# Kernel optimization log

Measured on AMD Instinct MI355X. Metric: run time of the kernel, lower is better.

The kernel has to match this reference:

```python
import jax, jax.numpy as jnp
import numpy as np
import math

B, S, D, H = 4, 2048, 1024, 16
DK = D // H  # 64
THETA = 10000.0


def setup_inputs() -> dict:
    key = jax.random.key(0)
    ks = jax.random.split(key, 5)
    std = 0.02
    return {
        "x": jax.random.normal(ks[0], (B, S, D), dtype=jnp.float32),
        "Wq": jax.random.normal(ks[1], (D, D), dtype=jnp.float32) * std,
        "Wk": jax.random.normal(ks[2], (D, D), dtype=jnp.float32) * std,
        "Wv": jax.random.normal(ks[3], (D, D), dtype=jnp.float32) * std,
        "Wo": jax.random.normal(ks[4], (D, D), dtype=jnp.float32) * std / math.sqrt(2 * 12),
        "token_positions": jnp.arange(S, dtype=jnp.int32),
    }


def _rope(x, pos):
    # x: [B, H, S, DK]; pos: [S]. Interleaved-pair rotary embedding.
    inv_freq = THETA ** (-jnp.arange(0, DK, 2, dtype=jnp.float32) / DK)  # [DK/2]
    ang = pos.astype(jnp.float32)[:, None] * inv_freq[None, :]  # [S, DK/2]
    cos, sin = jnp.cos(ang), jnp.sin(ang)
    x1, x2 = x[..., 0::2], x[..., 1::2]  # [B, H, S, DK/2]
    r1 = x1 * cos - x2 * sin
    r2 = x1 * sin + x2 * cos
    return jnp.stack([r1, r2], axis=-1).reshape(x.shape)


def reference(x, Wq, Wk, Wv, Wo, token_positions):
    b, s, d = x.shape
    Q = x @ Wq
    K = x @ Wk
    V = x @ Wv
    # [B, S, D] -> [B, H, S, DK]
    def split(t):
        return t.reshape(b, s, H, DK).transpose(0, 2, 1, 3)
    Qh, Kh, Vh = split(Q), split(K), split(V)
    Qh = _rope(Qh, token_positions)
    Kh = _rope(Kh, token_positions)
    scores = jnp.einsum('bhqd,bhkd->bhqk', Qh, Kh) / math.sqrt(DK)
    causal = jnp.tril(jnp.ones((s, s), dtype=bool))
    scores = jnp.where(causal, scores, -jnp.inf)
    probs = jax.nn.softmax(scores, axis=-1)
    out = jnp.einsum('bhqk,bhkd->bhqd', probs, Vh)
    out = out.transpose(0, 2, 1, 3).reshape(b, s, d)
    return out @ Wo
```

## Files before the change

### kernel.cpp

```cpp
#include <hip/hip_runtime.h>
#include <hip/hip_bf16.h>

#define B_N 4
#define S_LEN 2048
#define D_MODEL 1024
#define N_HEAD 16
#define D_HEAD 64
#define M_ROWS (B_N * S_LEN)

typedef short bf16x8 __attribute__((ext_vector_type(8)));
typedef short bf16x4 __attribute__((ext_vector_type(4)));
typedef float f32x4 __attribute__((ext_vector_type(4)));

#if __has_builtin(__builtin_amdgcn_mfma_f32_16x16x16bf16_1k)
#define HAVE_MFMA16 1
#else
#define HAVE_MFMA16 0
#endif

__device__ __forceinline__ unsigned short f2bf(float f) {
  union { float f; unsigned int u; } v; v.f = f;
  unsigned int r = v.u + 0x7FFFu + ((v.u >> 16) & 1u);
  return (unsigned short)(r >> 16);
}
__device__ __forceinline__ float bf2f(unsigned short u) {
  union { unsigned int u; float f; } v; v.u = ((unsigned int)u) << 16;
  return v.f;
}
__device__ __forceinline__ unsigned int pkbf(float a, float b) {
  union { __hip_bfloat162 h; unsigned int u; } cv;
  cv.h = __float22bfloat162_rn(make_float2(a, b));
  return cv.u;
}
__device__ __forceinline__ bf16x8 ld8(const unsigned short* p) {
  return *reinterpret_cast<const bf16x8*>(p);
}
__device__ __forceinline__ bf16x4 ld4(const unsigned short* p) {
  return *reinterpret_cast<const bf16x4*>(p);
}
__device__ __forceinline__ void glds16(const unsigned short* g, unsigned short* l) {
  __builtin_amdgcn_global_load_lds(
      (const __attribute__((address_space(1))) unsigned int*)g,
      (__attribute__((address_space(3))) unsigned int*)l, 16, 0, 0);
}

__global__ __launch_bounds__(256) void rope_tab_k(const int* __restrict__ pos,
                                                  float2* __restrict__ tab) {
  const int idx = blockIdx.x * 256 + threadIdx.x;
  const int s = idx >> 5;
  const int i = idx & 31;
  const float inv = exp2f(-(float)i * 0.41524101186092029f);
  const float ang = (float)pos[s] * inv;
  tab[idx] = make_float2(cosf(ang), sinf(ang));
}

__global__ __launch_bounds__(256) void cast_k(const float* __restrict__ X,
                                              unsigned short* __restrict__ Y) {
  const size_t i = ((size_t)blockIdx.x * 256 + threadIdx.x) * 8;
  const float4 a = *reinterpret_cast<const float4*>(X + i);
  const float4 b = *reinterpret_cast<const float4*>(X + i + 4);
  union { unsigned int u[4]; uint4 v; } o;
  o.u[0] = pkbf(a.x, a.y); o.u[1] = pkbf(a.z, a.w);
  o.u[2] = pkbf(b.x, b.y); o.u[3] = pkbf(b.z, b.w);
  *reinterpret_cast<uint4*>(Y + i) = o.v;
}

__global__ __launch_bounds__(256) void wtrans_k(
    const float* __restrict__ W0, const float* __restrict__ W1,
    const float* __restrict__ W2, const float* __restrict__ W3,
    unsigned short* __restrict__ T0, unsigned short* __restrict__ T1,
    unsigned short* __restrict__ T2, unsigned short* __restrict__ T3) {
  const int z = blockIdx.z;
  const float* __restrict__ W = (z == 0) ? W0 : (z == 1) ? W1 : (z == 2) ? W2 : W3;
  unsigned short* __restrict__ T = (z == 0) ? T0 : (z == 1) ? T1 : (z == 2) ? T2 : T3;
  __shared__ __align__(16) unsigned short tile[64][72];
  const int kb = blockIdx.x * 64;
  const int nb = blockIdx.y * 64;
#pragma unroll
  for (int it = 0; it < 2; ++it) {
    const int chunk = it * 256 + threadIdx.x;
    const int r = chunk >> 3;
    const int c8 = (chunk & 7) * 8;
    const float* src = W + (size_t)(kb + r) * D_MODEL + nb + c8;
    const float4 a = *reinterpret_cast<const float4*>(src);
    const float4 b = *reinterpret_cast<const float4*>(src + 4);
    union { unsigned int u[4]; uint4 v; } o;
    o.u[0] = pkbf(a.x, a.y); o.u[1] = pkbf(a.z, a.w);
    o.u[2] = pkbf(b.x, b.y); o.u[3] = pkbf(b.z, b.w);
    *reinterpret_cast<uint4*>(&tile[r][c8]) = o.v;
  }
  __syncthreads();
#pragma unroll
  for (int it = 0; it < 2; ++it) {
    const int chunk = it * 256 + threadIdx.x;
    const int n = chunk >> 3;
    const int k8 = (chunk & 7) * 8;
    __align__(16) unsigned short vals[8];
#pragma unroll
    for (int j = 0; j < 8; ++j) vals[j] = tile[k8 + j][n];
    *reinterpret_cast<uint4*>(T + (size_t)(nb + n) * D_MODEL + kb + k8) =
        *reinterpret_cast<const uint4*>(vals);
  }
}

__global__ __launch_bounds__(256) void gemm2_k(
    const unsigned short* __restrict__ A, const unsigned short* __restrict__ W,
    unsigned short* __restrict__ Qo, unsigned short* __restrict__ Ko,
    unsigned short* __restrict__ VTo, float* __restrict__ OF,
    const float2* __restrict__ tab, const int mode) {
  __shared__ __align__(16) unsigned short smem[4][64][68];
  unsigned short* As = &smem[0][0][0];
  unsigned short* Bs = As + 128 * 32;

  const int tid = threadIdx.x;
  const int lane = tid & 63;
  const int w = tid >> 6;
  const int l15 = lane & 15;
  const int l4 = lane >> 4;

  const int row0 = blockIdx.x * 128;
  const int col0 = blockIdx.y * 128;

  const int srow = w * 32 + (lane >> 2);
  const int scol = (lane & 3) * 8;
  const unsigned short* ga = A + (size_t)(row0 + srow) * D_MODEL + scol;
  const unsigned short* gb = W + (size_t)(col0 + srow) * D_MODEL + scol;
  unsigned short* la = &As[(w * 32) * 32];
  unsigned short* lb = &Bs[(w * 32) * 32];

  const int wrow = (w & 1) * 64;
  const int wcol = (w >> 1) * 64;

  f32x4 acc[4][4];
  const f32x4 fz = {0.f, 0.f, 0.f, 0.f};
#pragma unroll
  for (int m = 0; m < 4; ++m)
#pragma unroll
    for (int n = 0; n < 4; ++n) acc[m][n] = fz;

  for (int kb = 0; kb < D_MODEL; kb += 32) {
    glds16(ga + kb, la);
    glds16(ga + 16 * D_MODEL + kb, la + 16 * 32);
    glds16(gb + kb, lb);
    glds16(gb + 16 * D_MODEL + kb, lb + 16 * 32);
    __syncthreads();
    bf16x8 af[4], bfr[4];
#pragma unroll
    for (int m = 0; m < 4; ++m) af[m] = ld8(&As[(wrow + m * 16 + l15) * 32 + l4 * 8]);
#pragma unroll
    for (int n = 0; n < 4; ++n) bfr[n] = ld8(&Bs[(wcol + n * 16 + l15) * 32 + l4 * 8]);
#pragma unroll
    for (int m = 0; m < 4; ++m)
#pragma unroll
      for (int n = 0; n < 4; ++n)
        acc[m][n] = __builtin_amdgcn_mfma_f32_16x16x32_bf16(af[m], bfr[n], acc[m][n], 0, 0, 0);
    __syncthreads();
  }

  if (mode == 1) {
#pragma unroll
    for (int n = 0; n < 4; ++n) {
      const int gcol = col0 + wcol + n * 16 + l15;
#pragma unroll
      for (int m = 0; m < 4; ++m)
#pragma unroll
        for (int r = 0; r < 4; ++r)
          OF[(size_t)(row0 + wrow + m * 16 + l4 * 4 + r) * D_MODEL + gcol] = acc[m][n][r];
    }
    return;
  }

  unsigned short (*T)[68] = (unsigned short(*)[68]) & smem[w];
  const bool isV = (col0 >= 2048);
  if (!isV) {
#pragma unroll
    for (int m = 0; m < 4; ++m)
#pragma unroll
      for (int n = 0; n < 4; ++n)
#pragma unroll
        for (int r = 0; r < 4; ++r)
          T[m * 16 + l4 * 4 + r][n * 16 + l15] = f2bf(acc[m][n][r]);
  } else {
#pragma unroll
    for (int m = 0; m < 4; ++m)
#pragma unroll
      for (int n = 0; n < 4; ++n)
#pragma unroll
        for (int r = 0; r < 4; ++r)
          T[n * 16 + l15][m * 16 + l4 * 4 + r] = f2bf(acc[m][n][r]);
  }

  const int lr = lane >> 3;
  const int lc = lane & 7;
  if (!isV) {
    const bool isQ = (col0 < 1024);
    unsigned short* O = isQ ? Qo : Ko;
    const float qs = isQ ? 0.18033688011112042f : 1.0f;
    const int cbase = (col0 & 1023) + wcol;
#pragma unroll
    for (int rg = 0; rg < 8; ++rg) {
      const int trow = rg * 8 + lr;
      const int grow = row0 + wrow + trow;
      const int s = grow & (S_LEN - 1);
      const bf16x8 vv = ld8(&T[trow][lc * 8]);
      const float4 tA = *reinterpret_cast<const float4*>(&tab[s * 32 + lc * 4]);
      const float4 tB = *reinterpret_cast<const float4*>(&tab[s * 32 + lc * 4 + 2]);
      float x[8];
#pragma unroll
      for (int j = 0; j < 8; ++j) x[j] = bf2f((unsigned short)vv[j]);
      union { unsigned int u[4]; uint4 v; } o;
      o.u[0] = pkbf((x[0] * tA.x - x[1] * tA.y) * qs, (x[0] * tA.y + x[1] * tA.x) * qs);
      o.u[1] = pkbf((x[2] * tA.z - x[3] * tA.w) * qs, (x[2] * tA.w + x[3] * tA.z) * qs);
      o.u[2] = pkbf((x[4] * tB.x - x[5] * tB.y) * qs, (x[4] * tB.y + x[5] * tB.x) * qs);
      o.u[3] = pkbf((x[6] * tB.z - x[7] * tB.w) * qs, (x[6] * tB.w + x[7] * tB.z) * qs);
      *reinterpret_cast<uint4*>(O + (size_t)grow * D_MODEL + cbase + lc * 8) = o.v;
    }
  } else {
    const int vc0 = (col0 - 2048) + wcol;
    const int h = vc0 >> 6;
    const int b = row0 >> 11;
    const int s0 = (row0 & (S_LEN - 1)) + wrow;
#pragma unroll
    for (int rg = 0; rg < 8; ++rg) {
      const int dk = rg * 8 + lr;
      const bf16x8 vv = ld8(&T[dk][lc * 8]);
      *reinterpret_cast<bf16x8*>(
          VTo + ((size_t)((b << 4) + h) * 64 + dk) * S_LEN + s0 + lc * 8) = vv;
    }
  }
}

__global__ __launch_bounds__(512) void attn6_k(
    const unsigned short* __restrict__ Q, const unsigned short* __restrict__ K,
    const unsigned short* __restrict__ VT, unsigned short* __restrict__ O) {
  const int pair = blockIdx.x;
  const int h = blockIdx.y;
  const int b = blockIdx.z;
  const int tid = threadIdx.x;
  const int w = tid >> 6;
  const int lane = tid & 63;
  const int l15 = lane & 15;
  const int l4 = lane >> 4;

  __shared__ __align__(16) unsigned short Ks[64][72];
  __shared__ __align__(16) unsigned short Vs[64][72];
#if !HAVE_MFMA16
  __shared__ __align__(16) unsigned short Ps[8][16][72];
#endif

  const f32x4 fz = {0.f, 0.f, 0.f, 0.f};
  const unsigned short* kbase = K + (size_t)b * S_LEN * D_MODEL + h * D_HEAD;
  const unsigned short* vbase = VT + (size_t)((b << 4) + h) * 64 * S_LEN;

  const int rr = tid >> 3;
  const int c8 = (tid & 7) * 8;

  for (int half = 0; half < 2; ++half) {
    const int qt = half ? (15 - pair) : pair;
    const int qb = qt * 128;
    const int qw0 = qb + w * 16;

    bf16x8 qf[2];
#pragma unroll
    for (int kc = 0; kc < 2; ++kc)
      qf[kc] = ld8(Q + (size_t)(b * S_LEN + qw0 + l15) * D_MODEL +
                   h * D_HEAD + kc * 32 + l4 * 8);

    f32x4 o[4];
#pragma unroll
    for (int d = 0; d < 4; ++d) o[d] = fz;
    float lsum = 0.f;

    const int nkt = qb / 64 + 2;
    uint4 kreg = *reinterpret_cast<const uint4*>(kbase + (size_t)rr * D_MODEL + c8);
    uint4 vreg = *reinterpret_cast<const uint4*>(vbase + (size_t)rr * S_LEN + c8);

    for (int kt = 0; kt < nkt; ++kt) {
      const int kb0 = kt * 64;
      *reinterpret_cast<uint4*>(&Ks[rr][c8]) = kreg;
      *reinterpret_cast<uint4*>(&Vs[rr][c8]) = vreg;
      if (kt + 1 < nkt) {
        const int nb0 = kb0 + 64;
        kreg = *reinterpret_cast<const uint4*>(kbase + (size_t)(nb0 + rr) * D_MODEL + c8);
        vreg = *reinterpret_cast<const uint4*>(vbase + (size_t)rr * S_LEN + nb0 + c8);
      }
      __syncthreads();

      if (kb0 <= qw0 + 15) {
        f32x4 s[4];
#pragma unroll
        for (int n = 0; n < 4; ++n) {
          const bf16x8 kf0 = ld8(&Ks[n * 16 + l15][l4 * 8]);
          const bf16x8 kf1 = ld8(&Ks[n * 16 + l15][32 + l4 * 8]);
          f32x4 a0 = __builtin_amdgcn_mfma_f32_16x16x32_bf16(kf0, qf[0], fz, 0, 0, 0);
          s[n] = __builtin_amdgcn_mfma_f32_16x16x32_bf16(kf1, qf[1], a0, 0, 0, 0);
        }
        bf16x4 pf[4];
        const bool full = (kb0 + 63 <= qw0);
        const int q = qw0 + l15;
        float su = lsum;
#pragma unroll
        for (int n = 0; n < 4; ++n) {
          float e[4];
          if (full) {
#pragma unroll
            for (int r = 0; r < 4; ++r) e[r] = exp2f(s[n][r]);
          } else {
#pragma unroll
            for (int r = 0; r < 4; ++r) {
              const int key = kb0 + n * 16 + l4 * 4 + r;
              const float v = exp2f(s[n][r]);
              e[r] = (key <= q) ? v : 0.f;
            }
          }
          su += (e[0] + e[1]) + (e[2] + e[3]);
          union { unsigned int u[2]; bf16x4 v; } pk;
          pk.u[0] = pkbf(e[0], e[1]);
          pk.u[1] = pkbf(e[2], e[3]);
          pf[n] = pk.v;
        }
        lsum = su;

#if HAVE_MFMA16
#pragma unroll
        for (int d = 0; d < 4; ++d) {
          bf16x4 vfc[4];
#pragma unroll
          for (int c = 0; c < 4; ++c) vfc[c] = ld4(&Vs[d * 16 + l15][c * 16 + l4 * 4]);
#pragma unroll
          for (int c = 0; c < 4; ++c)
            o[d] = __builtin_amdgcn_mfma_f32_16x16x16bf16_1k(vfc[c], pf[c], o[d], 0, 0, 0);
        }
#else
#pragma unroll
        for (int n = 0; n < 4; ++n)
          *reinterpret_cast<bf16x4*>(&Ps[w][l15][n * 16 + l4 * 4]) = pf[n];
        bf16x8 pfr[2];
#pragma unroll
        for (int kc = 0; kc < 2; ++kc)
          pfr[kc] = ld8(&Ps[w][l15][kc * 32 + l4 * 8]);
#pragma unroll
        for (int d = 0; d < 4; ++d) {
          const bf16x8 vf0 = ld8(&Vs[d * 16 + l15][l4 * 8]);
          const bf16x8 vf1 = ld8(&Vs[d * 16 + l15][32 + l4 * 8]);
          o[d] = __builtin_amdgcn_mfma_f32_16x16x32_bf16(vf0, pfr[0], o[d], 0, 0, 0);
          o[d] = __builtin_amdgcn_mfma_f32_16x16x32_bf16(vf1, pfr[1], o[d], 0, 0, 0);
        }
#endif
      }
      __syncthreads();
    }

    float s = lsum;
    s += __shfl_xor(s, 16);
    s += __shfl_xor(s, 32);
    const float li = 1.0f / s;
    unsigned short* op = O + (size_t)(b * S_LEN + qw0 + l15) * D_MODEL +
                         h * D_HEAD + l4 * 4;
#pragma unroll
    for (int d = 0; d < 4; ++d) {
      union { unsigned int u[2]; uint2 v; } ov;
      ov.u[0] = pkbf(o[d][0] * li, o[d][1] * li);
      ov.u[1] = pkbf(o[d][2] * li, o[d][3] * li);
      *reinterpret_cast<uint2*>(op + d * 16) = ov.v;
    }
  }
}

extern "C" void kernel_launch(void* const* d_in, const int* in_sizes, int n_in,
                              void* d_out, int out_size, void* d_ws, size_t ws_size,
                              hipStream_t stream) {
  const float* x  = (const float*)d_in[0];
  const float* Wq = (const float*)d_in[1];
  const float* Wk = (const float*)d_in[2];
  const float* Wv = (const float*)d_in[3];
  const float* Wo = (const float*)d_in[4];
  const int* pos  = (const int*)d_in[5];
  float* out = (float*)d_out;

  char* ws = (char*)d_ws;
  const size_t big = (size_t)M_ROWS * D_MODEL * 2;
  const size_t wsz = (size_t)D_MODEL * D_MODEL * 2;
  unsigned short* xb  = (unsigned short*)(ws + 0 * big);
  unsigned short* Qb  = (unsigned short*)(ws + 1 * big);
  unsigned short* Kb  = (unsigned short*)(ws + 2 * big);
  unsigned short* VT  = (unsigned short*)(ws + 3 * big);
  unsigned short* Wqkvt = (unsigned short*)(ws + 4 * big);
  unsigned short* Wot   = (unsigned short*)(ws + 4 * big + 3 * wsz);
  float2* tab = (float2*)d_out;

  rope_tab_k<<<dim3(S_LEN * 32 / 256), 256, 0, stream>>>(pos, tab);
  cast_k<<<dim3(M_ROWS * D_MODEL / 2048), 256, 0, stream>>>(x, xb);
  wtrans_k<<<dim3(16, 16, 4), 256, 0, stream>>>(
      Wq, Wk, Wv, Wo, Wqkvt, Wqkvt + (size_t)D_MODEL * D_MODEL,
      Wqkvt + 2 * (size_t)D_MODEL * D_MODEL, Wot);
  gemm2_k<<<dim3(M_ROWS / 128, 3 * D_MODEL / 128), 256, 0, stream>>>(
      xb, Wqkvt, Qb, Kb, VT, nullptr, tab, 0);
  attn6_k<<<dim3(8, N_HEAD, B_N), 512, 0, stream>>>(Qb, Kb, VT, Qb);
  gemm2_k<<<dim3(M_ROWS / 128, D_MODEL / 128), 256, 0, stream>>>(
      Qb, Wot, nullptr, nullptr, nullptr, out, nullptr, 1);
}
```

Baseline: 277.9 us.

## Merge prep kernels into one launch and double attention KV tile to 128

Folds the rope table, input cast and weight transpose kernels into a single prep kernel that dispatches on block index, removing two launches. The attention kernel now stages 128 keys/values per iteration instead of 64 and processes them as two 64-key sub-tiles, halving the number of barrier pairs and global-load rounds. The larger tile raises LDS use per block and adds register pressure from the doubled prefetch registers.

```diff
diff --git a/kernel.cpp b/kernel.cpp
--- a/kernel.cpp
+++ b/kernel.cpp
@@ -44,62 +44,67 @@
       (__attribute__((address_space(3))) unsigned int*)l, 16, 0, 0);
 }
 
-__global__ __launch_bounds__(256) void rope_tab_k(const int* __restrict__ pos,
-                                                  float2* __restrict__ tab) {
-  const int idx = blockIdx.x * 256 + threadIdx.x;
-  const int s = idx >> 5;
-  const int i = idx & 31;
-  const float inv = exp2f(-(float)i * 0.41524101186092029f);
-  const float ang = (float)pos[s] * inv;
-  tab[idx] = make_float2(cosf(ang), sinf(ang));
-}
-
-__global__ __launch_bounds__(256) void cast_k(const float* __restrict__ X,
-                                              unsigned short* __restrict__ Y) {
-  const size_t i = ((size_t)blockIdx.x * 256 + threadIdx.x) * 8;
-  const float4 a = *reinterpret_cast<const float4*>(X + i);
-  const float4 b = *reinterpret_cast<const float4*>(X + i + 4);
-  union { unsigned int u[4]; uint4 v; } o;
-  o.u[0] = pkbf(a.x, a.y); o.u[1] = pkbf(a.z, a.w);
-  o.u[2] = pkbf(b.x, b.y); o.u[3] = pkbf(b.z, b.w);
-  *reinterpret_cast<uint4*>(Y + i) = o.v;
-}
-
-__global__ __launch_bounds__(256) void wtrans_k(
+__global__ __launch_bounds__(256) void prep_k(
+    const float* __restrict__ x,
     const float* __restrict__ W0, const float* __restrict__ W1,
     const float* __restrict__ W2, const float* __restrict__ W3,
+    const int* __restrict__ pos,
+    unsigned short* __restrict__ Y,
     unsigned short* __restrict__ T0, unsigned short* __restrict__ T1,
-    unsigned short* __restrict__ T2, unsigned short* __restrict__ T3) {
-  const int z = blockIdx.z;
-  const float* __restrict__ W = (z == 0) ? W0 : (z == 1) ? W1 : (z == 2) ? W2 : W3;
-  unsigned short* __restrict__ T = (z == 0) ? T0 : (z == 1) ? T1 : (z == 2) ? T2 : T3;
+    unsigned short* __restrict__ T2, unsigned short* __restrict__ T3,
+    float2* __restrict__ tab) {
   __shared__ __align__(16) unsigned short tile[64][72];
-  const int kb = blockIdx.x * 64;
-  const int nb = blockIdx.y * 64;
-#pragma unroll
-  for (int it = 0; it < 2; ++it) {
-    const int chunk = it * 256 + threadIdx.x;
-    const int r = chunk >> 3;
-    const int c8 = (chunk & 7) * 8;
-    const float* src = W + (size_t)(kb + r) * D_MODEL + nb + c8;
-    const float4 a = *reinterpret_cast<const float4*>(src);
-    const float4 b = *reinterpret_cast<const float4*>(src + 4);
+  const int blk = blockIdx.x;
+  const int tid = threadIdx.x;
+  if (blk < 4096) {
+    const size_t i = ((size_t)blk * 256 + tid) * 8;
+    const float4 a = *reinterpret_cast<const float4*>(x + i);
+    const float4 b = *reinterpret_cast<const float4*>(x + i + 4);
     union { unsigned int u[4]; uint4 v; } o;
     o.u[0] = pkbf(a.x, a.y); o.u[1] = pkbf(a.z, a.w);
     o.u[2] = pkbf(b.x, b.y); o.u[3] = pkbf(b.z, b.w);
-    *reinterpret_cast<uint4*>(&tile[r][c8]) = o.v;
-  }
-  __syncthreads();
-#pragma unroll
-  for (int it = 0; it < 2; ++it) {
-    const int chunk = it * 256 + threadIdx.x;
-    const int n = chunk >> 3;
-    const int k8 = (chunk & 7) * 8;
-    __align__(16) unsigned short vals[8];
-#pragma unroll
-    for (int j = 0; j < 8; ++j) vals[j] = tile[k8 + j][n];
-    *reinterpret_cast<uint4*>(T + (size_t)(nb + n) * D_MODEL + kb + k8) =
-        *reinterpret_cast<const uint4*>(vals);
+    *reinterpret_cast<uint4*>(Y + i) = o.v;
+  } else if (blk < 5120) {
+    const int linear = blk - 4096;
+    const int z = linear >> 8;
+    const int bx = linear & 15;
+    const int by = (linear >> 4) & 15;
+    const float* __restrict__ W = (z == 0) ? W0 : (z == 1) ? W1 : (z == 2) ? W2 : W3;
+    unsigned short* __restrict__ T = (z == 0) ? T0 : (z == 1) ? T1 : (z == 2) ? T2 : T3;
+    const int kb = bx * 64;
+    const int nb = by * 64;
+#pragma unroll
+    for (int it = 0; it < 2; ++it) {
+      const int chunk = it * 256 + tid;
+      const int r = chunk >> 3;
+      const int c8 = (chunk & 7) * 8;
+      const float* src = W + (size_t)(kb + r) * D_MODEL + nb + c8;
+      const float4 a = *reinterpret_cast<const float4*>(src);
+      const float4 b = *reinterpret_cast<const float4*>(src + 4);
+      union { unsigned int u[4]; uint4 v; } o;
+      o.u[0] = pkbf(a.x, a.y); o.u[1] = pkbf(a.z, a.w);
+      o.u[2] = pkbf(b.x, b.y); o.u[3] = pkbf(b.z, b.w);
+      *reinterpret_cast<uint4*>(&tile[r][c8]) = o.v;
+    }
+    __syncthreads();
+#pragma unroll
+    for (int it = 0; it < 2; ++it) {
+      const int chunk = it * 256 + tid;
+      const int n = chunk >> 3;
+      const int k8 = (chunk & 7) * 8;
+      __align__(16) unsigned short vals[8];
+#pragma unroll
+      for (int j = 0; j < 8; ++j) vals[j] = tile[k8 + j][n];
+      *reinterpret_cast<uint4*>(T + (size_t)(nb + n) * D_MODEL + kb + k8) =
+          *reinterpret_cast<const uint4*>(vals);
+    }
+  } else {
+    const int idx = (blk - 5120) * 256 + tid;
+    const int s = idx >> 5;
+    const int i = idx & 31;
+    const float inv = exp2f(-(float)i * 0.41524101186092029f);
+    const float ang = (float)pos[s] * inv;
+    tab[idx] = make_float2(cosf(ang), sinf(ang));
   }
 }
 
@@ -230,7 +235,7 @@
   }
 }
 
-__global__ __launch_bounds__(512) void attn6_k(
+__global__ __launch_bounds__(512) void attn7_k(
     const unsigned short* __restrict__ Q, const unsigned short* __restrict__ K,
     const unsigned short* __restrict__ VT, unsigned short* __restrict__ O) {
   const int pair = blockIdx.x;
@@ -242,8 +247,8 @@
   const int l15 = lane & 15;
   const int l4 = lane >> 4;
 
-  __shared__ __align__(16) unsigned short Ks[64][72];
-  __shared__ __align__(16) unsigned short Vs[64][72];
+  __shared__ __align__(16) unsigned short Ks[128][72];
+  __shared__ __align__(16) unsigned short Vs[64][136];
 #if !HAVE_MFMA16
   __shared__ __align__(16) unsigned short Ps[8][16][72];
 #endif
@@ -252,8 +257,10 @@
   const unsigned short* kbase = K + (size_t)b * S_LEN * D_MODEL + h * D_HEAD;
   const unsigned short* vbase = VT + (size_t)((b << 4) + h) * 64 * S_LEN;
 
-  const int rr = tid >> 3;
-  const int c8 = (tid & 7) * 8;
+  const int krr = tid >> 3;
+  const int kc8 = (tid & 7) * 8;
+  const int vrr = tid >> 4;
+  const int vc8 = (tid & 15) * 8;
 
   for (int half = 0; half < 2; ++half) {
     const int qt = half ? (15 - pair) : pair;
@@ -271,82 +278,97 @@
     for (int d = 0; d < 4; ++d) o[d] = fz;
     float lsum = 0.f;
 
-    const int nkt = qb / 64 + 2;
-    uint4 kreg = *reinterpret_cast<const uint4*>(kbase + (size_t)rr * D_MODEL + c8);
-    uint4 vreg = *reinterpret_cast<const uint4*>(vbase + (size_t)rr * S_LEN + c8);
+    const int nkt = qt + 1;
+    uint4 kreg[2], vreg[2];
+#pragma unroll
+    for (int p = 0; p < 2; ++p) {
+      kreg[p] = *reinterpret_cast<const uint4*>(kbase + (size_t)(p * 64 + krr) * D_MODEL + kc8);
+      vreg[p] = *reinterpret_cast<const uint4*>(vbase + (size_t)(p * 32 + vrr) * S_LEN + vc8);
+    }
 
     for (int kt = 0; kt < nkt; ++kt) {
-      const int kb0 = kt * 64;
-      *reinterpret_cast<uint4*>(&Ks[rr][c8]) = kreg;
-      *reinterpret_cast<uint4*>(&Vs[rr][c8]) = vreg;
+      const int kb0 = kt * 128;
+#pragma unroll
+      for (int p = 0; p < 2; ++p) {
+        *reinterpret_cast<uint4*>(&Ks[p * 64 + krr][kc8]) = kreg[p];
+        *reinterpret_cast<uint4*>(&Vs[p * 32 + vrr][vc8]) = vreg[p];
+      }
       if (kt + 1 < nkt) {
-        const int nb0 = kb0 + 64;
-        kreg = *reinterpret_cast<const uint4*>(kbase + (size_t)(nb0 + rr) * D_MODEL + c8);
-        vreg = *reinterpret_cast<const uint4*>(vbase + (size_t)rr * S_LEN + nb0 + c8);
+        const int nb0 = kb0 + 128;
+#pragma unroll
+        for (int p = 0; p < 2; ++p) {
+          kreg[p] = *reinterpret_cast<const uint4*>(kbase + (size_t)(nb0 + p * 64 + krr) * D_MODEL + kc8);
+          vreg[p] = *reinterpret_cast<const uint4*>(vbase + (size_t)(p * 32 + vrr) * S_LEN + nb0 + vc8);
+        }
       }
       __syncthreads();
 
-      if (kb0 <= qw0 + 15) {
-        f32x4 s[4];
-#pragma unroll
-        for (int n = 0; n < 4; ++n) {
-          const bf16x8 kf0 = ld8(&Ks[n * 16 + l15][l4 * 8]);
-          const bf16x8 kf1 = ld8(&Ks[n * 16 + l15][32 + l4 * 8]);
-          f32x4 a0 = __builtin_amdgcn_mfma_f32_16x16x32_bf16(kf0, qf[0], fz, 0, 0, 0);
-          s[n] = __builtin_amdgcn_mfma_f32_16x16x32_bf16(kf1, qf[1], a0, 0, 0, 0);
+#pragma unroll
+      for (int sub = 0; sub < 2; ++sub) {
+        const int kbs = kb0 + sub * 64;
+        if (kbs <= qw0 + 15) {
+          f32x4 s[4];
+#pragma unroll
+          for (int n = 0; n < 4; ++n) {
+            const bf16x8 kf0 = ld8(&Ks[sub * 64 + n * 16 + l15][l4 * 8]);
+            const bf16x8 kf1 = ld8(&Ks[sub * 64 + n * 16 + l15][32 + l4 * 8]);
+            f32x4 a0 = __builtin_amdgcn_mfma_f32_16x16x32_bf16(kf0, qf[0], fz, 0, 0, 0);
+            s[n] = __builtin_amdgcn_mfma_f32_16x16x32_bf16(kf1, qf[1], a0, 0, 0, 0);
+          }
+          bf16x4 pf[4];
+          const bool full = (kbs + 63 <= qw0);
+          const int q = qw0 + l15;
+          float su = lsum;
+#pragma unroll
+          for (int n = 0; n < 4; ++n) {
+            float e[4];
+            if (full) {
+#pragma unroll
+              for (int r = 0; r < 4; ++r) e[r] = exp2f(s[n][r]);
+            } else {
+#pragma unroll
+              for (int r = 0; r < 4; ++r) {
+                const int key = kbs + n * 16 + l4 * 4 + r;
+                const float v = exp2f(s[n][r]);
+                e[r] = (key <= q) ? v : 0.f;
+              }
+            }
+            su += (e[0] + e[1]) + (e[2] + e[3]);
+            union { unsigned int u[2]; bf16x4 v; } pk;
+            pk.u[0] = pkbf(e[0], e[1]);
+            pk.u[1] = pkbf(e[2], e[3]);
+            pf[n] = pk.v;
+          }
+          lsum = su;
+
+#if HAVE_MFMA16
+#pragma unroll
+          for (int d = 0; d < 4; ++d) {
+            bf16x4 vfc[4];
+#pragma unroll
+            for (int c = 0; c < 4; ++c)
+              vfc[c] = ld4(&Vs[d * 16 + l15][sub * 64 + c * 16 + l4 * 4]);
+#pragma unroll
+            for (int c = 0; c < 4; ++c)
+              o[d] = __builtin_amdgcn_mfma_f32_16x16x16bf16_1k(vfc[c], pf[c], o[d], 0, 0, 0);
+          }
+#else
+#pragma unroll
+          for (int n = 0; n < 4; ++n)
+            *reinterpret_cast<bf16x4*>(&Ps[w][l15][n * 16 + l4 * 4]) = pf[n];
+          bf16x8 pfr[2];
+#pragma unroll
+          for (int kc = 0; kc < 2; ++kc)
+            pfr[kc] = ld8(&Ps[w][l15][kc * 32 + l4 * 8]);
+#pragma unroll
+          for (int d = 0; d < 4; ++d) {
+            const bf16x8 vf0 = ld8(&Vs[d * 16 + l15][sub * 64 + l4 * 8]);
+            const bf16x8 vf1 = ld8(&Vs[d * 16 + l15][sub * 64 + 32 + l4 * 8]);
+            o[d] = __builtin_amdgcn_mfma_f32_16x16x32_bf16(vf0, pfr[0], o[d], 0, 0, 0);
+            o[d] = __builtin_amdgcn_mfma_f32_16x16x32_bf16(vf1, pfr[1], o[d], 0, 0, 0);
+          }
+#endif
         }
-        bf16x4 pf[4];
-        const bool full = (kb0 + 63 <= qw0);
-        const int q = qw0 + l15;
-        float su = lsum;
-#pragma unroll
-        for (int n = 0; n < 4; ++n) {
-          float e[4];
-          if (full) {
-#pragma unroll
-            for (int r = 0; r < 4; ++r) e[r] = exp2f(s[n][r]);
-          } else {
-#pragma unroll
-            for (int r = 0; r < 4; ++r) {
-              const int key = kb0 + n * 16 + l4 * 4 + r;
-              const float v = exp2f(s[n][r]);
-              e[r] = (key <= q) ? v : 0.f;
-            }
-          }
-          su += (e[0] + e[1]) + (e[2] + e[3]);
-          union { unsigned int u[2]; bf16x4 v; } pk;
-          pk.u[0] = pkbf(e[0], e[1]);
-          pk.u[1] = pkbf(e[2], e[3]);
-          pf[n] = pk.v;
-        }
-        lsum = su;
-
-#if HAVE_MFMA16
-#pragma unroll
-        for (int d = 0; d < 4; ++d) {
-          bf16x4 vfc[4];
-#pragma unroll
-          for (int c = 0; c < 4; ++c) vfc[c] = ld4(&Vs[d * 16 + l15][c * 16 + l4 * 4]);
-#pragma unroll
-          for (int c = 0; c < 4; ++c)
-            o[d] = __builtin_amdgcn_mfma_f32_16x16x16bf16_1k(vfc[c], pf[c], o[d], 0, 0, 0);
-        }
-#else
-#pragma unroll
-        for (int n = 0; n < 4; ++n)
-          *reinterpret_cast<bf16x4*>(&Ps[w][l15][n * 16 + l4 * 4]) = pf[n];
-        bf16x8 pfr[2];
-#pragma unroll
-        for (int kc = 0; kc < 2; ++kc)
-          pfr[kc] = ld8(&Ps[w][l15][kc * 32 + l4 * 8]);
-#pragma unroll
-        for (int d = 0; d < 4; ++d) {
-          const bf16x8 vf0 = ld8(&Vs[d * 16 + l15][l4 * 8]);
-          const bf16x8 vf1 = ld8(&Vs[d * 16 + l15][32 + l4 * 8]);
-          o[d] = __builtin_amdgcn_mfma_f32_16x16x32_bf16(vf0, pfr[0], o[d], 0, 0, 0);
-          o[d] = __builtin_amdgcn_mfma_f32_16x16x32_bf16(vf1, pfr[1], o[d], 0, 0, 0);
-        }
-#endif
       }
       __syncthreads();
     }
@@ -389,14 +411,13 @@
   unsigned short* Wot   = (unsigned short*)(ws + 4 * big + 3 * wsz);
   float2* tab = (float2*)d_out;
 
-  rope_tab_k<<<dim3(S_LEN * 32 / 256), 256, 0, stream>>>(pos, tab);
-  cast_k<<<dim3(M_ROWS * D_MODEL / 2048), 256, 0, stream>>>(x, xb);
-  wtrans_k<<<dim3(16, 16, 4), 256, 0, stream>>>(
-      Wq, Wk, Wv, Wo, Wqkvt, Wqkvt + (size_t)D_MODEL * D_MODEL,
-      Wqkvt + 2 * (size_t)D_MODEL * D_MODEL, Wot);
+  prep_k<<<dim3(5376), 256, 0, stream>>>(
+      x, Wq, Wk, Wv, Wo, pos, xb,
+      Wqkvt, Wqkvt + (size_t)D_MODEL * D_MODEL,
+      Wqkvt + 2 * (size_t)D_MODEL * D_MODEL, Wot, tab);
   gemm2_k<<<dim3(M_ROWS / 128, 3 * D_MODEL / 128), 256, 0, stream>>>(
       xb, Wqkvt, Qb, Kb, VT, nullptr, tab, 0);
-  attn6_k<<<dim3(8, N_HEAD, B_N), 512, 0, stream>>>(Qb, Kb, VT, Qb);
+  attn7_k<<<dim3(8, N_HEAD, B_N), 512, 0, stream>>>(Qb, Kb, VT, Qb);
   gemm2_k<<<dim3(M_ROWS / 128, D_MODEL / 128), 256, 0, stream>>>(
       Qb, Wot, nullptr, nullptr, nullptr, out, nullptr, 1);
 }
```

After: 321.5 us. 1.16x slower.
